# Kernel tuning notes

Measured on AMD Instinct MI355X. Metric: run time of the kernel, lower is better.

Reference implementation:

```python
import jax, jax.numpy as jnp
import numpy as np
import math

NUM_HEADS = 16
LOGIT_SCALE_MAX = math.log(1.0 / 0.01)  # log(100)
EPS = 1e-12


def _l2norm(x):
    # F.normalize(x, dim=-1): x / max(||x||_2, eps)
    n = jnp.sqrt(jnp.sum(x * x, axis=-1, keepdims=True))
    return x / jnp.maximum(n, EPS)


def setup_inputs() -> dict:
    key = jax.random.key(0)
    ks = jax.random.split(key, 6)
    N, B, C = 1024, 4, 1024
    scale = (C // NUM_HEADS) ** -0.5
    return {
        "query": jax.random.normal(ks[0], (N, B, C), jnp.float32),
        "key": jax.random.normal(ks[1], (N, B, C), jnp.float32),
        "value": jax.random.normal(ks[2], (N, B, C), jnp.float32),
        "in_proj_w": jax.random.normal(ks[3], (3 * C, C), jnp.float32) * scale,
        "in_proj_b": jnp.zeros((3 * C,), jnp.float32),
        "logit_scale": jnp.log(10.0) * jnp.ones((NUM_HEADS, 1, 1), jnp.float32),
        "out_w": jax.random.normal(ks[4], (C, C), jnp.float32) * scale,
        "out_b": jnp.zeros((C,), jnp.float32),
    }


def reference(query, key, value, in_proj_w, in_proj_b, logit_scale, out_w, out_b):
    N, B, C = query.shape
    H = NUM_HEADS
    hd = C // H
    # packed in-projection, split into q/k/v pieces
    w_q, w_k, w_v = jnp.split(in_proj_w, 3, axis=0)
    b_q, b_k, b_v = jnp.split(in_proj_b, 3, axis=0)
    q = query @ w_q.T + b_q          # (N, B, C)
    k = key @ w_k.T + b_k
    v = value @ w_v.T + b_v
    # (N, B, C) -> (B*H, N, hd)
    q = q.reshape(N, B * H, hd).swapaxes(0, 1)
    k = k.reshape(N, B * H, hd).swapaxes(0, 1)
    v = v.reshape(N, B * H, hd).swapaxes(0, 1)
    # cosine-similarity scores with learnable per-head logit scale
    attn = jnp.einsum('bqd,bkd->bqk', _l2norm(q), _l2norm(k))  # (B*H, N, N)
    ls = jnp.exp(jnp.minimum(logit_scale, LOGIT_SCALE_MAX))     # (H,1,1)
    attn = (attn.reshape(B, H, N, N) * ls).reshape(B * H, N, N)
    attn = jax.nn.softmax(attn, axis=-1)
    x = jnp.einsum('bqk,bkd->bqd', attn, v)                     # (B*H, N, hd)
    x = x.swapaxes(0, 1).reshape(N, B, C)
    return x @ out_w.T + out_b
```

## Files before the change

kernel.cpp:

```cpp
#include <hip/hip_runtime.h>


typedef _Float16 f16x8 __attribute__((ext_vector_type(8)));
typedef __fp16   h16x2 __attribute__((ext_vector_type(2)));
typedef float    f32x4 __attribute__((ext_vector_type(4)));

#define LOG2E 1.4426950408889634f
#define LOGMAX 4.6051702f

#define GLOAD16(g, l) \
    __builtin_amdgcn_global_load_lds((__attribute__((address_space(1))) void*)(g), \
                                     (__attribute__((address_space(3))) void*)(l), 16, 0, 0)

__device__ __forceinline__ unsigned short f2h(float x) {
    union { _Float16 h; unsigned short u; } cv;
    cv.h = (_Float16)x;
    return cv.u;
}

__global__ __launch_bounds__(256) void cvt_all(
    const float* __restrict__ q, const float* __restrict__ k,
    const float* __restrict__ v, const float* __restrict__ w,
    const float* __restrict__ ow,
    unsigned short* __restrict__ qbf, unsigned short* __restrict__ kbf,
    unsigned short* __restrict__ vbf, unsigned short* __restrict__ wbf,
    unsigned short* __restrict__ owbf)
{
    int b = blockIdx.x;
    const float* src; unsigned short* dst; int idx;
    if      (b < 4096)  { src = q;  dst = qbf;  idx = b; }
    else if (b < 8192)  { src = k;  dst = kbf;  idx = b - 4096; }
    else if (b < 12288) { src = v;  dst = vbf;  idx = b - 8192; }
    else if (b < 15360) { src = w;  dst = wbf;  idx = b - 12288; }
    else                { src = ow; dst = owbf; idx = b - 15360; }
    int i = idx * 256 + threadIdx.x;
    float4 val = ((const float4*)src)[i];
    ushort4 o;
    o.x = f2h(val.x); o.y = f2h(val.y); o.z = f2h(val.z); o.w = f2h(val.w);
    ((ushort4*)dst)[i] = o;
}

__global__ __launch_bounds__(256) void proj_gemm(
    const unsigned short* __restrict__ qbf, const unsigned short* __restrict__ kbf,
    const unsigned short* __restrict__ vbf, const unsigned short* __restrict__ wbf,
    const float* __restrict__ bias, const float* __restrict__ lsc,
    unsigned short* __restrict__ qn, unsigned short* __restrict__ kn,
    unsigned short* __restrict__ vT)
{
    __shared__ __align__(16) unsigned short AsmF[128 * 64];
    __shared__ __align__(16) unsigned short BsmF[128 * 64];
    int tid = threadIdx.x;
    int lane = tid & 63, wave = tid >> 6;
    int lr = lane & 15, lq = lane >> 4;
    int wr = wave >> 1, wc = wave & 1;

    int lin = blockIdx.x;
    int xcd = lin & 7, s = lin >> 3;
    int xt = s & 7, yy = (s >> 3) & 3, z = s >> 5;
    int m0 = (xcd * 4 + yy) * 128, n0 = xt * 128;

    const unsigned short* A = (z == 0) ? qbf : (z == 1) ? kbf : vbf;
    const unsigned short* W = wbf + (size_t)z * 1024 * 1024;

    int rl = lane >> 3;
    int cg = ((lane & 7) ^ rl) << 3;
    const unsigned short* gA = A + (size_t)(m0 + wave * 32 + rl) * 1024 + cg;
    const unsigned short* gB = W + (size_t)(n0 + wave * 32 + rl) * 1024 + cg;
    unsigned short* lA = &AsmF[wave * 32 * 64];
    unsigned short* lB = &BsmF[wave * 32 * 64];

    int swz = lr & 7;
    int c0 = (lq ^ swz) << 3;
    int c1 = ((lq ^ 4) ^ swz) << 3;

    f32x4 acc[4][4];
    for (int i = 0; i < 4; i++) for (int j = 0; j < 4; j++) acc[i][j] = (f32x4){0.f, 0.f, 0.f, 0.f};

    for (int ki = 0; ki < 16; ++ki) {
        for (int j = 0; j < 4; ++j) {
            GLOAD16(gA + ki * 64 + j * 8192, lA + j * 512);
            GLOAD16(gB + ki * 64 + j * 8192, lB + j * 512);
        }
        __syncthreads();
        for (int kc = 0; kc < 2; ++kc) {
            int co = kc ? c1 : c0;
            f16x8 af[4], bfr[4];
            for (int mi = 0; mi < 4; ++mi) af[mi]  = *(const f16x8*)&AsmF[(wr * 64 + mi * 16 + lr) * 64 + co];
            for (int ni = 0; ni < 4; ++ni) bfr[ni] = *(const f16x8*)&BsmF[(wc * 64 + ni * 16 + lr) * 64 + co];
            for (int mi = 0; mi < 4; ++mi)
                for (int ni = 0; ni < 4; ++ni)
                    acc[mi][ni] = __builtin_amdgcn_mfma_f32_16x16x32_f16(af[mi], bfr[ni], acc[mi][ni], 0, 0, 0);
        }
        __syncthreads();
    }

    int h = (n0 >> 6) + wc;
    float bv[4];
    for (int ni = 0; ni < 4; ++ni) bv[ni] = bias[z * 1024 + n0 + wc * 64 + ni * 16 + lr];
    for (int mi = 0; mi < 4; ++mi)
        for (int ni = 0; ni < 4; ++ni)
            for (int r = 0; r < 4; ++r) acc[mi][ni][r] += bv[ni];

    float lsfac = __expf(fminf(lsc[h], LOGMAX)) * LOG2E;

    for (int mi = 0; mi < 4; ++mi)
        for (int r = 0; r < 4; ++r) {
            int row = m0 + wr * 64 + mi * 16 + lq * 4 + r;
            int n = row >> 2, b = row & 3;
            int bh = b * 16 + h;
            if (z < 2) {
                float ss = 0.f;
                for (int ni = 0; ni < 4; ++ni) ss += acc[mi][ni][r] * acc[mi][ni][r];
                for (int off = 1; off < 16; off <<= 1) ss += __shfl_xor(ss, off);
                float scale = 1.0f / fmaxf(sqrtf(ss), 1e-12f);
                if (z == 0) scale *= lsfac;
                unsigned short* dst = (z == 0) ? qn : kn;
                for (int ni = 0; ni < 4; ++ni)
                    dst[(size_t)bh * 65536 + (size_t)n * 64 + ni * 16 + lr] = f2h(acc[mi][ni][r] * scale);
            } else {
                for (int ni = 0; ni < 4; ++ni)
                    vT[(size_t)bh * 65536 + (size_t)(ni * 16 + lr) * 1024 + n] = f2h(acc[mi][ni][r]);
            }
        }
}

__global__ __launch_bounds__(256) void flash_kernel(
    const unsigned short* __restrict__ qn, const unsigned short* __restrict__ kn,
    const unsigned short* __restrict__ vT, const float* __restrict__ lsc,
    unsigned short* __restrict__ xb)
{
    __shared__ __align__(16) unsigned short K_flat[64 * 64];
    __shared__ __align__(16) unsigned short V_flat[64 * 64];
    __shared__ __align__(16) unsigned short P_lds[4][16][72];
    int tid = threadIdx.x;
    int lane = tid & 63, wave = tid >> 6;
    int lr = lane & 15, lq = lane >> 4;

    int lin = blockIdx.x;
    int xcd = lin & 7, s = lin >> 3;
    int qt = s & 15, bh = xcd * 8 + (s >> 4);
    int q0 = qt * 64;

    float off = __expf(fminf(lsc[bh & 15], LOGMAX)) * LOG2E - 12.0f;
    f32x4 initv = (f32x4){-off, -off, -off, -off};

    f16x8 qf[2];
    for (int kc = 0; kc < 2; ++kc)
        qf[kc] = *(const f16x8*)(qn + (size_t)bh * 65536 +
                      (size_t)(q0 + wave * 16 + lr) * 64 + kc * 32 + lq * 8);

    int rl = lane >> 3;
    int cg = ((lane & 7) ^ rl) << 3;
    const unsigned short* gK = kn + (size_t)bh * 65536 + (size_t)(wave * 16 + rl) * 64 + cg;
    const unsigned short* gV = vT + (size_t)bh * 65536 + (size_t)(wave * 16 + rl) * 1024 + cg;
    unsigned short* lK = &K_flat[wave * 16 * 64];
    unsigned short* lV = &V_flat[wave * 16 * 64];
    int swz = lr & 7;
    int c0 = (lq ^ swz) << 3;
    int c1 = ((lq ^ 4) ^ swz) << 3;

    f32x4 o[4];
    for (int i = 0; i < 4; i++) o[i] = (f32x4){0.f, 0.f, 0.f, 0.f};
    float lsum = 0.f;

    for (int kt = 0; kt < 16; ++kt) {
        for (int j = 0; j < 2; ++j) {
            GLOAD16(gK + kt * 4096 + j * 512,  lK + j * 512);
            GLOAD16(gV + kt * 64  + j * 8192,  lV + j * 512);
        }
        __syncthreads();

        f32x4 sc[4];
        __builtin_amdgcn_s_setprio(1);
        for (int ct = 0; ct < 4; ++ct)
            for (int kc = 0; kc < 2; ++kc) {
                f16x8 kf = *(const f16x8*)&K_flat[(ct * 16 + lr) * 64 + (kc ? c1 : c0)];
                sc[ct] = __builtin_amdgcn_mfma_f32_16x16x32_f16(
                    kf, qf[kc], kc == 0 ? initv : sc[ct], 0, 0, 0);
            }
        __builtin_amdgcn_s_setprio(0);

        for (int ct = 0; ct < 4; ++ct) {
            float p0 = __builtin_amdgcn_exp2f(sc[ct][0]);
            float p1 = __builtin_amdgcn_exp2f(sc[ct][1]);
            float p2 = __builtin_amdgcn_exp2f(sc[ct][2]);
            float p3 = __builtin_amdgcn_exp2f(sc[ct][3]);
            lsum += (p0 + p1) + (p2 + p3);
            union { h16x2 h[2]; ushort4 u; } pw;
            pw.h[0] = __builtin_amdgcn_cvt_pkrtz(p0, p1);
            pw.h[1] = __builtin_amdgcn_cvt_pkrtz(p2, p3);
            *(ushort4*)&P_lds[wave][lr][ct * 16 + lq * 4] = pw.u;
        }

        f16x8 pf[2];
        for (int kc = 0; kc < 2; ++kc)
            pf[kc] = *(const f16x8*)&P_lds[wave][lr][kc * 32 + lq * 8];
        __builtin_amdgcn_s_setprio(1);
        for (int nt = 0; nt < 4; ++nt)
            for (int kc = 0; kc < 2; ++kc) {
                f16x8 vf = *(const f16x8*)&V_flat[(nt * 16 + lr) * 64 + (kc ? c1 : c0)];
                o[nt] = __builtin_amdgcn_mfma_f32_16x16x32_f16(vf, pf[kc], o[nt], 0, 0, 0);
            }
        __builtin_amdgcn_s_setprio(0);
        __syncthreads();
    }

    int b = bh >> 4, h = bh & 15;
    float ls = lsum;
    ls += __shfl_xor(ls, 16);
    ls += __shfl_xor(ls, 32);
    float inv = 1.0f / ls;
    size_t m = (size_t)(q0 + wave * 16 + lr) * 4 + b;
    for (int nt = 0; nt < 4; ++nt) {
        ushort4 w;
        w.x = f2h(o[nt][0] * inv); w.y = f2h(o[nt][1] * inv);
        w.z = f2h(o[nt][2] * inv); w.w = f2h(o[nt][3] * inv);
        *(ushort4*)(xb + m * 1024 + h * 64 + nt * 16 + lq * 4) = w;
    }
}

__global__ __launch_bounds__(256) void out_gemm(
    const unsigned short* __restrict__ xb, const unsigned short* __restrict__ owbf,
    const float* __restrict__ bias, float* __restrict__ outp)
{
    __shared__ __align__(16) unsigned short AsmF[128 * 64];
    __shared__ __align__(16) unsigned short BsmF[64 * 64];
    int tid = threadIdx.x;
    int lane = tid & 63, wave = tid >> 6;
    int lr = lane & 15, lq = lane >> 4;

    int lin = blockIdx.x;
    int xcd = lin & 7, s = lin >> 3;
    int xt = s & 15, yy = s >> 4;
    int m0 = (xcd * 4 + yy) * 128, n0 = xt * 64;

    int rl = lane >> 3;
    int cg = ((lane & 7) ^ rl) << 3;
    const unsigned short* gA = xb   + (size_t)(m0 + wave * 32 + rl) * 1024 + cg;
    const unsigned short* gB = owbf + (size_t)(n0 + wave * 16 + rl) * 1024 + cg;
    unsigned short* lA = &AsmF[wave * 32 * 64];
    unsigned short* lB = &BsmF[wave * 16 * 64];
    int swz = lr & 7;
    int c0 = (lq ^ swz) << 3;
    int c1 = ((lq ^ 4) ^ swz) << 3;

    f32x4 acc[2][4];
    for (int i = 0; i < 2; i++) for (int j = 0; j < 4; j++) acc[i][j] = (f32x4){0.f, 0.f, 0.f, 0.f};

    for (int ki = 0; ki < 16; ++ki) {
        for (int j = 0; j < 4; ++j)
            GLOAD16(gA + ki * 64 + j * 8192, lA + j * 512);
        for (int j = 0; j < 2; ++j)
            GLOAD16(gB + ki * 64 + j * 8192, lB + j * 512);
        __syncthreads();
        for (int kc = 0; kc < 2; ++kc) {
            int co = kc ? c1 : c0;
            f16x8 af[2], bfr[4];
            for (int mi = 0; mi < 2; ++mi) af[mi]  = *(const f16x8*)&AsmF[(wave * 32 + mi * 16 + lr) * 64 + co];
            for (int ni = 0; ni < 4; ++ni) bfr[ni] = *(const f16x8*)&BsmF[(ni * 16 + lr) * 64 + co];
            for (int mi = 0; mi < 2; ++mi)
                for (int ni = 0; ni < 4; ++ni)
                    acc[mi][ni] = __builtin_amdgcn_mfma_f32_16x16x32_f16(af[mi], bfr[ni], acc[mi][ni], 0, 0, 0);
        }
        __syncthreads();
    }
    for (int mi = 0; mi < 2; ++mi)
        for (int ni = 0; ni < 4; ++ni)
            for (int r = 0; r < 4; ++r) {
                int row = m0 + wave * 32 + mi * 16 + lq * 4 + r;
                int col = n0 + ni * 16 + lr;
                outp[(size_t)row * 1024 + col] = acc[mi][ni][r] + bias[col];
            }
}

extern "C" void kernel_launch(void* const* d_in, const int* in_sizes, int n_in,
                              void* d_out, int out_size, void* d_ws, size_t ws_size,
                              hipStream_t stream) {
    const float* query = (const float*)d_in[0];
    const float* key   = (const float*)d_in[1];
    const float* value = (const float*)d_in[2];
    const float* ipw   = (const float*)d_in[3];
    const float* ipb   = (const float*)d_in[4];
    const float* lsc   = (const float*)d_in[5];
    const float* ow    = (const float*)d_in[6];
    const float* ob    = (const float*)d_in[7];
    float* outp = (float*)d_out;

    char* ws = (char*)d_ws;
    unsigned short* qbf  = (unsigned short*)(ws);
    unsigned short* kbf  = (unsigned short*)(ws + 8388608);
    unsigned short* vbf  = (unsigned short*)(ws + 16777216);
    unsigned short* wbf  = (unsigned short*)(ws + 25165824);
    unsigned short* owbf = (unsigned short*)(ws + 31457280);
    unsigned short* qn   = (unsigned short*)(ws + 33554432);
    unsigned short* kn   = (unsigned short*)(ws + 41943040);
    unsigned short* vT   = (unsigned short*)(ws + 50331648);
    unsigned short* xbuf = (unsigned short*)(ws + 58720256);

    cvt_all<<<16384, 256, 0, stream>>>(query, key, value, ipw, ow,
                                       qbf, kbf, vbf, wbf, owbf);
    proj_gemm<<<768, 256, 0, stream>>>(qbf, kbf, vbf, wbf, ipb, lsc, qn, kn, vT);
    flash_kernel<<<1024, 256, 0, stream>>>(qn, kn, vT, lsc, xbuf);
    out_gemm<<<512, 256, 0, stream>>>(xbuf, owbf, ob, outp);
}
```

Before: 202.0 us.

## Fuse all four stages into one persistent kernel with grid barriers

Replaces the four separate launches (convert, projection GEMM, flash attention, output GEMM) with one persistent 1024-block kernel. The stages are separated by a software grid barrier built on a global atomic counter, and all stages share one LDS buffer. The aim is to remove the launch gaps and tail drain between kernels. In exchange it needs all 1024 blocks to be resident at once and adds spin-wait barrier cost. Its timeout guard could break out early and silently give wrong results.

```diff
diff --git a/kernel.cpp b/kernel.cpp
--- a/kernel.cpp
+++ b/kernel.cpp
@@ -18,259 +18,260 @@
     return cv.u;
 }
 
-__global__ __launch_bounds__(256) void cvt_all(
+__device__ unsigned long long g_cnt;
+
+__device__ __forceinline__ void grid_bar(unsigned long long target) {
+    __syncthreads();
+    if (threadIdx.x == 0) {
+        __threadfence();
+        atomicAdd(&g_cnt, 1ull);
+        long long guard = 0;
+        while (__hip_atomic_load(&g_cnt, __ATOMIC_RELAXED, __HIP_MEMORY_SCOPE_AGENT) < target) {
+            __builtin_amdgcn_s_sleep(2);
+            if (++guard > (1ll << 24)) break;
+        }
+        __threadfence();
+    }
+    __syncthreads();
+}
+
+__global__ __launch_bounds__(256, 4) void mega(
     const float* __restrict__ q, const float* __restrict__ k,
     const float* __restrict__ v, const float* __restrict__ w,
-    const float* __restrict__ ow,
+    const float* __restrict__ ow, const float* __restrict__ ipb,
+    const float* __restrict__ lsc, const float* __restrict__ ob,
     unsigned short* __restrict__ qbf, unsigned short* __restrict__ kbf,
     unsigned short* __restrict__ vbf, unsigned short* __restrict__ wbf,
-    unsigned short* __restrict__ owbf)
+    unsigned short* __restrict__ owbf,
+    unsigned short* __restrict__ qn, unsigned short* __restrict__ kn,
+    unsigned short* __restrict__ vT, unsigned short* __restrict__ xb,
+    float* __restrict__ outp)
 {
-    int b = blockIdx.x;
-    const float* src; unsigned short* dst; int idx;
-    if      (b < 4096)  { src = q;  dst = qbf;  idx = b; }
-    else if (b < 8192)  { src = k;  dst = kbf;  idx = b - 4096; }
-    else if (b < 12288) { src = v;  dst = vbf;  idx = b - 8192; }
-    else if (b < 15360) { src = w;  dst = wbf;  idx = b - 12288; }
-    else                { src = ow; dst = owbf; idx = b - 15360; }
-    int i = idx * 256 + threadIdx.x;
-    float4 val = ((const float4*)src)[i];
-    ushort4 o;
-    o.x = f2h(val.x); o.y = f2h(val.y); o.z = f2h(val.z); o.w = f2h(val.w);
-    ((ushort4*)dst)[i] = o;
-}
-
-__global__ __launch_bounds__(256) void proj_gemm(
-    const unsigned short* __restrict__ qbf, const unsigned short* __restrict__ kbf,
-    const unsigned short* __restrict__ vbf, const unsigned short* __restrict__ wbf,
-    const float* __restrict__ bias, const float* __restrict__ lsc,
-    unsigned short* __restrict__ qn, unsigned short* __restrict__ kn,
-    unsigned short* __restrict__ vT)
-{
-    __shared__ __align__(16) unsigned short AsmF[128 * 64];
-    __shared__ __align__(16) unsigned short BsmF[128 * 64];
-    int tid = threadIdx.x;
-    int lane = tid & 63, wave = tid >> 6;
-    int lr = lane & 15, lq = lane >> 4;
-    int wr = wave >> 1, wc = wave & 1;
-
-    int lin = blockIdx.x;
-    int xcd = lin & 7, s = lin >> 3;
-    int xt = s & 7, yy = (s >> 3) & 3, z = s >> 5;
-    int m0 = (xcd * 4 + yy) * 128, n0 = xt * 128;
-
-    const unsigned short* A = (z == 0) ? qbf : (z == 1) ? kbf : vbf;
-    const unsigned short* W = wbf + (size_t)z * 1024 * 1024;
-
-    int rl = lane >> 3;
-    int cg = ((lane & 7) ^ rl) << 3;
-    const unsigned short* gA = A + (size_t)(m0 + wave * 32 + rl) * 1024 + cg;
-    const unsigned short* gB = W + (size_t)(n0 + wave * 32 + rl) * 1024 + cg;
-    unsigned short* lA = &AsmF[wave * 32 * 64];
-    unsigned short* lB = &BsmF[wave * 32 * 64];
-
-    int swz = lr & 7;
-    int c0 = (lq ^ swz) << 3;
-    int c1 = ((lq ^ 4) ^ swz) << 3;
-
-    f32x4 acc[4][4];
-    for (int i = 0; i < 4; i++) for (int j = 0; j < 4; j++) acc[i][j] = (f32x4){0.f, 0.f, 0.f, 0.f};
-
-    for (int ki = 0; ki < 16; ++ki) {
-        for (int j = 0; j < 4; ++j) {
-            GLOAD16(gA + ki * 64 + j * 8192, lA + j * 512);
-            GLOAD16(gB + ki * 64 + j * 8192, lB + j * 512);
-        }
-        __syncthreads();
-        for (int kc = 0; kc < 2; ++kc) {
-            int co = kc ? c1 : c0;
-            f16x8 af[4], bfr[4];
-            for (int mi = 0; mi < 4; ++mi) af[mi]  = *(const f16x8*)&AsmF[(wr * 64 + mi * 16 + lr) * 64 + co];
-            for (int ni = 0; ni < 4; ++ni) bfr[ni] = *(const f16x8*)&BsmF[(wc * 64 + ni * 16 + lr) * 64 + co];
-            for (int mi = 0; mi < 4; ++mi)
-                for (int ni = 0; ni < 4; ++ni)
-                    acc[mi][ni] = __builtin_amdgcn_mfma_f32_16x16x32_f16(af[mi], bfr[ni], acc[mi][ni], 0, 0, 0);
-        }
-        __syncthreads();
-    }
-
-    int h = (n0 >> 6) + wc;
-    float bv[4];
-    for (int ni = 0; ni < 4; ++ni) bv[ni] = bias[z * 1024 + n0 + wc * 64 + ni * 16 + lr];
-    for (int mi = 0; mi < 4; ++mi)
-        for (int ni = 0; ni < 4; ++ni)
-            for (int r = 0; r < 4; ++r) acc[mi][ni][r] += bv[ni];
-
-    float lsfac = __expf(fminf(lsc[h], LOGMAX)) * LOG2E;
-
-    for (int mi = 0; mi < 4; ++mi)
-        for (int r = 0; r < 4; ++r) {
-            int row = m0 + wr * 64 + mi * 16 + lq * 4 + r;
-            int n = row >> 2, b = row & 3;
-            int bh = b * 16 + h;
-            if (z < 2) {
-                float ss = 0.f;
-                for (int ni = 0; ni < 4; ++ni) ss += acc[mi][ni][r] * acc[mi][ni][r];
-                for (int off = 1; off < 16; off <<= 1) ss += __shfl_xor(ss, off);
-                float scale = 1.0f / fmaxf(sqrtf(ss), 1e-12f);
-                if (z == 0) scale *= lsfac;
-                unsigned short* dst = (z == 0) ? qn : kn;
-                for (int ni = 0; ni < 4; ++ni)
-                    dst[(size_t)bh * 65536 + (size_t)n * 64 + ni * 16 + lr] = f2h(acc[mi][ni][r] * scale);
-            } else {
-                for (int ni = 0; ni < 4; ++ni)
-                    vT[(size_t)bh * 65536 + (size_t)(ni * 16 + lr) * 1024 + n] = f2h(acc[mi][ni][r]);
-            }
-        }
-}
-
-__global__ __launch_bounds__(256) void flash_kernel(
-    const unsigned short* __restrict__ qn, const unsigned short* __restrict__ kn,
-    const unsigned short* __restrict__ vT, const float* __restrict__ lsc,
-    unsigned short* __restrict__ xb)
-{
-    __shared__ __align__(16) unsigned short K_flat[64 * 64];
-    __shared__ __align__(16) unsigned short V_flat[64 * 64];
-    __shared__ __align__(16) unsigned short P_lds[4][16][72];
-    int tid = threadIdx.x;
-    int lane = tid & 63, wave = tid >> 6;
-    int lr = lane & 15, lq = lane >> 4;
-
-    int lin = blockIdx.x;
-    int xcd = lin & 7, s = lin >> 3;
-    int qt = s & 15, bh = xcd * 8 + (s >> 4);
-    int q0 = qt * 64;
-
-    float off = __expf(fminf(lsc[bh & 15], LOGMAX)) * LOG2E - 12.0f;
-    f32x4 initv = (f32x4){-off, -off, -off, -off};
-
-    f16x8 qf[2];
-    for (int kc = 0; kc < 2; ++kc)
-        qf[kc] = *(const f16x8*)(qn + (size_t)bh * 65536 +
-                      (size_t)(q0 + wave * 16 + lr) * 64 + kc * 32 + lq * 8);
-
-    int rl = lane >> 3;
-    int cg = ((lane & 7) ^ rl) << 3;
-    const unsigned short* gK = kn + (size_t)bh * 65536 + (size_t)(wave * 16 + rl) * 64 + cg;
-    const unsigned short* gV = vT + (size_t)bh * 65536 + (size_t)(wave * 16 + rl) * 1024 + cg;
-    unsigned short* lK = &K_flat[wave * 16 * 64];
-    unsigned short* lV = &V_flat[wave * 16 * 64];
-    int swz = lr & 7;
-    int c0 = (lq ^ swz) << 3;
-    int c1 = ((lq ^ 4) ^ swz) << 3;
-
-    f32x4 o[4];
-    for (int i = 0; i < 4; i++) o[i] = (f32x4){0.f, 0.f, 0.f, 0.f};
-    float lsum = 0.f;
-
-    for (int kt = 0; kt < 16; ++kt) {
-        for (int j = 0; j < 2; ++j) {
-            GLOAD16(gK + kt * 4096 + j * 512,  lK + j * 512);
-            GLOAD16(gV + kt * 64  + j * 8192,  lV + j * 512);
-        }
-        __syncthreads();
-
-        f32x4 sc[4];
-        __builtin_amdgcn_s_setprio(1);
-        for (int ct = 0; ct < 4; ++ct)
+    __shared__ __align__(16) unsigned short smem[16384];
+    const int tid = threadIdx.x;
+    const int bid = blockIdx.x;
+    const int lane = tid & 63, wave = tid >> 6;
+    const int lr = lane & 15, lq = lane >> 4;
+
+    unsigned long long base = 0;
+    if (tid == 0)
+        base = (__hip_atomic_load(&g_cnt, __ATOMIC_RELAXED, __HIP_MEMORY_SCOPE_AGENT) / 3072ull) * 3072ull;
+
+    for (int vb = bid; vb < 16384; vb += 1024) {
+        const float* src; unsigned short* dst; int idx;
+        if      (vb < 4096)  { src = q;  dst = qbf;  idx = vb; }
+        else if (vb < 8192)  { src = k;  dst = kbf;  idx = vb - 4096; }
+        else if (vb < 12288) { src = v;  dst = vbf;  idx = vb - 8192; }
+        else if (vb < 15360) { src = w;  dst = wbf;  idx = vb - 12288; }
+        else                 { src = ow; dst = owbf; idx = vb - 15360; }
+        int i = idx * 256 + tid;
+        float4 val = ((const float4*)src)[i];
+        ushort4 o;
+        o.x = f2h(val.x); o.y = f2h(val.y); o.z = f2h(val.z); o.w = f2h(val.w);
+        ((ushort4*)dst)[i] = o;
+    }
+    grid_bar(base + 1024);
+
+    if (bid < 768) {
+        int wr = wave >> 1, wc = wave & 1;
+        int xcd = bid & 7, s = bid >> 3;
+        int xt = s & 7, yy = (s >> 3) & 3, z = s >> 5;
+        int m0 = (xcd * 4 + yy) * 128, n0 = xt * 128;
+
+        const unsigned short* A = (z == 0) ? qbf : (z == 1) ? kbf : vbf;
+        const unsigned short* W = wbf + (size_t)z * 1048576;
+
+        int rl = lane >> 3;
+        int cg = ((lane & 7) ^ rl) << 3;
+        const unsigned short* gA = A + (size_t)(m0 + wave * 32 + rl) * 1024 + cg;
+        const unsigned short* gB = W + (size_t)(n0 + wave * 32 + rl) * 1024 + cg;
+        unsigned short* lA = &smem[wave * 2048];
+        unsigned short* lB = &smem[8192 + wave * 2048];
+
+        int swz = lr & 7;
+        int c0 = (lq ^ swz) << 3;
+        int c1 = ((lq ^ 4) ^ swz) << 3;
+
+        f32x4 acc[4][4];
+        for (int i = 0; i < 4; i++) for (int j = 0; j < 4; j++) acc[i][j] = (f32x4){0.f, 0.f, 0.f, 0.f};
+
+        for (int ki = 0; ki < 16; ++ki) {
+            for (int j = 0; j < 4; ++j) {
+                GLOAD16(gA + ki * 64 + j * 8192, lA + j * 512);
+                GLOAD16(gB + ki * 64 + j * 8192, lB + j * 512);
+            }
+            __syncthreads();
             for (int kc = 0; kc < 2; ++kc) {
-                f16x8 kf = *(const f16x8*)&K_flat[(ct * 16 + lr) * 64 + (kc ? c1 : c0)];
-                sc[ct] = __builtin_amdgcn_mfma_f32_16x16x32_f16(
-                    kf, qf[kc], kc == 0 ? initv : sc[ct], 0, 0, 0);
-            }
-        __builtin_amdgcn_s_setprio(0);
-
-        for (int ct = 0; ct < 4; ++ct) {
-            float p0 = __builtin_amdgcn_exp2f(sc[ct][0]);
-            float p1 = __builtin_amdgcn_exp2f(sc[ct][1]);
-            float p2 = __builtin_amdgcn_exp2f(sc[ct][2]);
-            float p3 = __builtin_amdgcn_exp2f(sc[ct][3]);
-            lsum += (p0 + p1) + (p2 + p3);
-            union { h16x2 h[2]; ushort4 u; } pw;
-            pw.h[0] = __builtin_amdgcn_cvt_pkrtz(p0, p1);
-            pw.h[1] = __builtin_amdgcn_cvt_pkrtz(p2, p3);
-            *(ushort4*)&P_lds[wave][lr][ct * 16 + lq * 4] = pw.u;
-        }
-
-        f16x8 pf[2];
+                int co = kc ? c1 : c0;
+                f16x8 af[4], bfr[4];
+                for (int mi = 0; mi < 4; ++mi) af[mi]  = *(const f16x8*)&smem[(wr * 64 + mi * 16 + lr) * 64 + co];
+                for (int ni = 0; ni < 4; ++ni) bfr[ni] = *(const f16x8*)&smem[8192 + (wc * 64 + ni * 16 + lr) * 64 + co];
+                for (int mi = 0; mi < 4; ++mi)
+                    for (int ni = 0; ni < 4; ++ni)
+                        acc[mi][ni] = __builtin_amdgcn_mfma_f32_16x16x32_f16(af[mi], bfr[ni], acc[mi][ni], 0, 0, 0);
+            }
+            __syncthreads();
+        }
+
+        int h = (n0 >> 6) + wc;
+        float bv[4];
+        for (int ni = 0; ni < 4; ++ni) bv[ni] = ipb[z * 1024 + n0 + wc * 64 + ni * 16 + lr];
+        for (int mi = 0; mi < 4; ++mi)
+            for (int ni = 0; ni < 4; ++ni)
+                for (int r = 0; r < 4; ++r) acc[mi][ni][r] += bv[ni];
+
+        float lsfac = __expf(fminf(lsc[h], LOGMAX)) * LOG2E;
+
+        for (int mi = 0; mi < 4; ++mi)
+            for (int r = 0; r < 4; ++r) {
+                int row = m0 + wr * 64 + mi * 16 + lq * 4 + r;
+                int n = row >> 2, b = row & 3;
+                int bh = b * 16 + h;
+                if (z < 2) {
+                    float ss = 0.f;
+                    for (int ni = 0; ni < 4; ++ni) ss += acc[mi][ni][r] * acc[mi][ni][r];
+                    for (int off = 1; off < 16; off <<= 1) ss += __shfl_xor(ss, off);
+                    float scale = 1.0f / fmaxf(sqrtf(ss), 1e-12f);
+                    if (z == 0) scale *= lsfac;
+                    unsigned short* dst = (z == 0) ? qn : kn;
+                    for (int ni = 0; ni < 4; ++ni)
+                        dst[(size_t)bh * 65536 + (size_t)n * 64 + ni * 16 + lr] = f2h(acc[mi][ni][r] * scale);
+                } else {
+                    for (int ni = 0; ni < 4; ++ni)
+                        vT[(size_t)bh * 65536 + (size_t)(ni * 16 + lr) * 1024 + n] = f2h(acc[mi][ni][r]);
+                }
+            }
+    }
+    grid_bar(base + 2048);
+
+    {
+        int xcd = bid & 7, s2 = bid >> 3;
+        int qt = s2 & 15, bh = xcd * 8 + (s2 >> 4);
+        int q0 = qt * 64;
+
+        float offv = __expf(fminf(lsc[bh & 15], LOGMAX)) * LOG2E - 12.0f;
+        f32x4 initv = (f32x4){-offv, -offv, -offv, -offv};
+
+        f16x8 qf[2];
         for (int kc = 0; kc < 2; ++kc)
-            pf[kc] = *(const f16x8*)&P_lds[wave][lr][kc * 32 + lq * 8];
-        __builtin_amdgcn_s_setprio(1);
-        for (int nt = 0; nt < 4; ++nt)
+            qf[kc] = *(const f16x8*)(qn + (size_t)bh * 65536 +
+                          (size_t)(q0 + wave * 16 + lr) * 64 + kc * 32 + lq * 8);
+
+        int rl = lane >> 3;
+        int cg = ((lane & 7) ^ rl) << 3;
+        const unsigned short* gK = kn + (size_t)bh * 65536 + (size_t)(wave * 16 + rl) * 64 + cg;
+        const unsigned short* gV = vT + (size_t)bh * 65536 + (size_t)(wave * 16 + rl) * 1024 + cg;
+        unsigned short* lK = &smem[wave * 1024];
+        unsigned short* lV = &smem[4096 + wave * 1024];
+        unsigned short* Pl = &smem[8192];
+        int swz = lr & 7;
+        int c0 = (lq ^ swz) << 3;
+        int c1 = ((lq ^ 4) ^ swz) << 3;
+
+        f32x4 o4[4];
+        for (int i = 0; i < 4; i++) o4[i] = (f32x4){0.f, 0.f, 0.f, 0.f};
+        float lsum = 0.f;
+
+        for (int kt = 0; kt < 16; ++kt) {
+            for (int j = 0; j < 2; ++j) {
+                GLOAD16(gK + kt * 4096 + j * 512,  lK + j * 512);
+                GLOAD16(gV + kt * 64  + j * 8192,  lV + j * 512);
+            }
+            __syncthreads();
+
+            f32x4 sc[4];
+            __builtin_amdgcn_s_setprio(1);
+            for (int ct = 0; ct < 4; ++ct)
+                for (int kc = 0; kc < 2; ++kc) {
+                    f16x8 kf = *(const f16x8*)&smem[(ct * 16 + lr) * 64 + (kc ? c1 : c0)];
+                    sc[ct] = __builtin_amdgcn_mfma_f32_16x16x32_f16(
+                        kf, qf[kc], kc == 0 ? initv : sc[ct], 0, 0, 0);
+                }
+            __builtin_amdgcn_s_setprio(0);
+
+            for (int ct = 0; ct < 4; ++ct) {
+                float p0 = __builtin_amdgcn_exp2f(sc[ct][0]);
+                float p1 = __builtin_amdgcn_exp2f(sc[ct][1]);
+                float p2 = __builtin_amdgcn_exp2f(sc[ct][2]);
+                float p3 = __builtin_amdgcn_exp2f(sc[ct][3]);
+                lsum += (p0 + p1) + (p2 + p3);
+                union { h16x2 h[2]; ushort4 u; } pw;
+                pw.h[0] = __builtin_amdgcn_cvt_pkrtz(p0, p1);
+                pw.h[1] = __builtin_amdgcn_cvt_pkrtz(p2, p3);
+                *(ushort4*)&Pl[(wave * 16 + lr) * 72 + ct * 16 + lq * 4] = pw.u;
+            }
+
+            f16x8 pf[2];
+            for (int kc = 0; kc < 2; ++kc)
+                pf[kc] = *(const f16x8*)&Pl[(wave * 16 + lr) * 72 + kc * 32 + lq * 8];
+            __builtin_amdgcn_s_setprio(1);
+            for (int nt = 0; nt < 4; ++nt)
+                for (int kc = 0; kc < 2; ++kc) {
+                    f16x8 vf = *(const f16x8*)&smem[4096 + (nt * 16 + lr) * 64 + (kc ? c1 : c0)];
+                    o4[nt] = __builtin_amdgcn_mfma_f32_16x16x32_f16(vf, pf[kc], o4[nt], 0, 0, 0);
+                }
+            __builtin_amdgcn_s_setprio(0);
+            __syncthreads();
+        }
+
+        int b = bh >> 4, h = bh & 15;
+        float ls = lsum;
+        ls += __shfl_xor(ls, 16);
+        ls += __shfl_xor(ls, 32);
+        float inv = 1.0f / ls;
+        size_t m = (size_t)(q0 + wave * 16 + lr) * 4 + b;
+        for (int nt = 0; nt < 4; ++nt) {
+            ushort4 wv;
+            wv.x = f2h(o4[nt][0] * inv); wv.y = f2h(o4[nt][1] * inv);
+            wv.z = f2h(o4[nt][2] * inv); wv.w = f2h(o4[nt][3] * inv);
+            *(ushort4*)(xb + m * 1024 + h * 64 + nt * 16 + lq * 4) = wv;
+        }
+    }
+    grid_bar(base + 3072);
+
+    if (bid < 512) {
+        int xcd = bid & 7, s3 = bid >> 3;
+        int xt = s3 & 15, yy = s3 >> 4;
+        int m0 = (xcd * 4 + yy) * 128, n0 = xt * 64;
+
+        int rl = lane >> 3;
+        int cg = ((lane & 7) ^ rl) << 3;
+        const unsigned short* gA = xb   + (size_t)(m0 + wave * 32 + rl) * 1024 + cg;
+        const unsigned short* gB = owbf + (size_t)(n0 + wave * 16 + rl) * 1024 + cg;
+        unsigned short* lA = &smem[wave * 2048];
+        unsigned short* lB = &smem[8192 + wave * 1024];
+        int swz = lr & 7;
+        int c0 = (lq ^ swz) << 3;
+        int c1 = ((lq ^ 4) ^ swz) << 3;
+
+        f32x4 acc[2][4];
+        for (int i = 0; i < 2; i++) for (int j = 0; j < 4; j++) acc[i][j] = (f32x4){0.f, 0.f, 0.f, 0.f};
+
+        for (int ki = 0; ki < 16; ++ki) {
+            for (int j = 0; j < 4; ++j)
+                GLOAD16(gA + ki * 64 + j * 8192, lA + j * 512);
+            for (int j = 0; j < 2; ++j)
+                GLOAD16(gB + ki * 64 + j * 8192, lB + j * 512);
+            __syncthreads();
             for (int kc = 0; kc < 2; ++kc) {
-                f16x8 vf = *(const f16x8*)&V_flat[(nt * 16 + lr) * 64 + (kc ? c1 : c0)];
-                o[nt] = __builtin_amdgcn_mfma_f32_16x16x32_f16(vf, pf[kc], o[nt], 0, 0, 0);
-            }
-        __builtin_amdgcn_s_setprio(0);
-        __syncthreads();
-    }
-
-    int b = bh >> 4, h = bh & 15;
-    float ls = lsum;
-    ls += __shfl_xor(ls, 16);
-    ls += __shfl_xor(ls, 32);
-    float inv = 1.0f / ls;
-    size_t m = (size_t)(q0 + wave * 16 + lr) * 4 + b;
-    for (int nt = 0; nt < 4; ++nt) {
-        ushort4 w;
-        w.x = f2h(o[nt][0] * inv); w.y = f2h(o[nt][1] * inv);
-        w.z = f2h(o[nt][2] * inv); w.w = f2h(o[nt][3] * inv);
-        *(ushort4*)(xb + m * 1024 + h * 64 + nt * 16 + lq * 4) = w;
-    }
-}
-
-__global__ __launch_bounds__(256) void out_gemm(
-    const unsigned short* __restrict__ xb, const unsigned short* __restrict__ owbf,
-    const float* __restrict__ bias, float* __restrict__ outp)
-{
-    __shared__ __align__(16) unsigned short AsmF[128 * 64];
-    __shared__ __align__(16) unsigned short BsmF[64 * 64];
-    int tid = threadIdx.x;
-    int lane = tid & 63, wave = tid >> 6;
-    int lr = lane & 15, lq = lane >> 4;
-
-    int lin = blockIdx.x;
-    int xcd = lin & 7, s = lin >> 3;
-    int xt = s & 15, yy = s >> 4;
-    int m0 = (xcd * 4 + yy) * 128, n0 = xt * 64;
-
-    int rl = lane >> 3;
-    int cg = ((lane & 7) ^ rl) << 3;
-    const unsigned short* gA = xb   + (size_t)(m0 + wave * 32 + rl) * 1024 + cg;
-    const unsigned short* gB = owbf + (size_t)(n0 + wave * 16 + rl) * 1024 + cg;
-    unsigned short* lA = &AsmF[wave * 32 * 64];
-    unsigned short* lB = &BsmF[wave * 16 * 64];
-    int swz = lr & 7;
-    int c0 = (lq ^ swz) << 3;
-    int c1 = ((lq ^ 4) ^ swz) << 3;
-
-    f32x4 acc[2][4];
-    for (int i = 0; i < 2; i++) for (int j = 0; j < 4; j++) acc[i][j] = (f32x4){0.f, 0.f, 0.f, 0.f};
-
-    for (int ki = 0; ki < 16; ++ki) {
-        for (int j = 0; j < 4; ++j)
-            GLOAD16(gA + ki * 64 + j * 8192, lA + j * 512);
-        for (int j = 0; j < 2; ++j)
-            GLOAD16(gB + ki * 64 + j * 8192, lB + j * 512);
-        __syncthreads();
-        for (int kc = 0; kc < 2; ++kc) {
-            int co = kc ? c1 : c0;
-            f16x8 af[2], bfr[4];
-            for (int mi = 0; mi < 2; ++mi) af[mi]  = *(const f16x8*)&AsmF[(wave * 32 + mi * 16 + lr) * 64 + co];
-            for (int ni = 0; ni < 4; ++ni) bfr[ni] = *(const f16x8*)&BsmF[(ni * 16 + lr) * 64 + co];
-            for (int mi = 0; mi < 2; ++mi)
-                for (int ni = 0; ni < 4; ++ni)
-                    acc[mi][ni] = __builtin_amdgcn_mfma_f32_16x16x32_f16(af[mi], bfr[ni], acc[mi][ni], 0, 0, 0);
-        }
-        __syncthreads();
-    }
-    for (int mi = 0; mi < 2; ++mi)
-        for (int ni = 0; ni < 4; ++ni)
-            for (int r = 0; r < 4; ++r) {
-                int row = m0 + wave * 32 + mi * 16 + lq * 4 + r;
-                int col = n0 + ni * 16 + lr;
-                outp[(size_t)row * 1024 + col] = acc[mi][ni][r] + bias[col];
-            }
+                int co = kc ? c1 : c0;
+                f16x8 af[2], bfr[4];
+                for (int mi = 0; mi < 2; ++mi) af[mi]  = *(const f16x8*)&smem[(wave * 32 + mi * 16 + lr) * 64 + co];
+                for (int ni = 0; ni < 4; ++ni) bfr[ni] = *(const f16x8*)&smem[8192 + (ni * 16 + lr) * 64 + co];
+                for (int mi = 0; mi < 2; ++mi)
+                    for (int ni = 0; ni < 4; ++ni)
+                        acc[mi][ni] = __builtin_amdgcn_mfma_f32_16x16x32_f16(af[mi], bfr[ni], acc[mi][ni], 0, 0, 0);
+            }
+            __syncthreads();
+        }
+        for (int mi = 0; mi < 2; ++mi)
+            for (int ni = 0; ni < 4; ++ni)
+                for (int r = 0; r < 4; ++r) {
+                    int row = m0 + wave * 32 + mi * 16 + lq * 4 + r;
+                    int col = n0 + ni * 16 + lr;
+                    outp[(size_t)row * 1024 + col] = acc[mi][ni][r] + ob[col];
+                }
+    }
 }
 
 extern "C" void kernel_launch(void* const* d_in, const int* in_sizes, int n_in,
@@ -297,9 +298,7 @@
     unsigned short* vT   = (unsigned short*)(ws + 50331648);
     unsigned short* xbuf = (unsigned short*)(ws + 58720256);
 
-    cvt_all<<<16384, 256, 0, stream>>>(query, key, value, ipw, ow,
-                                       qbf, kbf, vbf, wbf, owbf);
-    proj_gemm<<<768, 256, 0, stream>>>(qbf, kbf, vbf, wbf, ipb, lsc, qn, kn, vT);
-    flash_kernel<<<1024, 256, 0, stream>>>(qn, kn, vT, lsc, xbuf);
-    out_gemm<<<512, 256, 0, stream>>>(xbuf, owbf, ob, outp);
+    mega<<<1024, 256, 0, stream>>>(query, key, value, ipw, ow, ipb, lsc, ob,
+                                   qbf, kbf, vbf, wbf, owbf,
+                                   qn, kn, vT, xbuf, outp);
 }
```

Result: slower. 550.8 us (+172.7%).
